# Optimization experiments

Measured on AMD Instinct MI355X. Metric: run time of the kernel, lower is better.

The kernel has to match this reference:

```python
import jax, jax.numpy as jnp
import numpy as np

SCALE_FACTORS = (1, 2, 4)
N, T, F = 4096, 128, 128
MARKET = 64
MIX = sum(T // k for k in SCALE_FACTORS)  # 224


def hardswish(x):
    return x * jnp.clip(x + 3.0, 0.0, 6.0) * (1.0 / 6.0)


def layernorm2d(x, g, b, eps=1e-5):
    # LayerNorm with normalized_shape == last two dims (as in torch nn.LayerNorm((A, B)))
    mu = jnp.mean(x, axis=(-2, -1), keepdims=True)
    var = jnp.var(x, axis=(-2, -1), keepdims=True)
    return (x - mu) * jax.lax.rsqrt(var + eps) * g + b


def setup_inputs() -> dict:
    key = jax.random.key(0)
    ks = jax.random.split(key, 32)
    inp = {"x": jax.random.normal(ks[0], (N, T, F), jnp.float32)}
    i = 1
    for si, k in enumerate(SCALE_FACTORS):
        tk = T // k
        inp[f"cw{si}"] = jax.random.normal(ks[i], (F, F, k), jnp.float32) * 0.05; i += 1
        inp[f"cb{si}"] = jnp.zeros((F,), jnp.float32)
        inp[f"lg{si}"] = jnp.ones((tk, F), jnp.float32)
        inp[f"lb{si}"] = jnp.zeros((tk, F), jnp.float32)
        inp[f"L1_{si}"] = jax.random.normal(ks[i], (tk, tk), jnp.float32) * 0.01; i += 1
        inp[f"L2_{si}"] = jax.random.normal(ks[i], (tk, tk), jnp.float32) * 0.01; i += 1
    inp["fc_w"] = jax.random.normal(ks[i], (1, F), jnp.float32) * 0.05; i += 1
    inp["fc_b"] = jnp.zeros((1,), jnp.float32)
    inp["sm_lg"] = jnp.ones((N, MIX), jnp.float32)
    inp["sm_lb"] = jnp.zeros((N, MIX), jnp.float32)
    inp["M1"] = jax.random.normal(ks[i], (MARKET, N), jnp.float32); i += 1
    inp["M2"] = jax.random.normal(ks[i], (N, MARKET), jnp.float32); i += 1
    inp["sm_fc_w"] = jax.random.normal(ks[i], (1, 2 * MIX), jnp.float32) * 0.02; i += 1
    inp["sm_fc_b"] = jnp.zeros((1,), jnp.float32)
    return inp


def _forward(x, cw0, cb0, lg0, lb0, L1_0, L2_0,
             cw1, cb1, lg1, lb1, L1_1, L2_1,
             cw2, cb2, lg2, lb2, L1_2, L2_2,
             fc_w, fc_b, sm_lg, sm_lb, M1, M2, sm_fc_w, sm_fc_b):
    n, t, f = x.shape
    per_scale = ((cw0, cb0, lg0, lb0, L1_0, L2_0),
                 (cw1, cb1, lg1, lb1, L1_1, L2_1),
                 (cw2, cb2, lg2, lb2, L1_2, L2_2))
    parts = []
    for k, (cw, cb, lg, lb, L1, L2) in zip(SCALE_FACTORS, per_scale):
        tk = t // k
        # Conv1d(kernel=k, stride=k) == blockwise contraction over non-overlapping windows
        xr = x.transpose(0, 2, 1).reshape(n, f, tk, k)          # (n, F_in, tk, k)
        xt = jnp.einsum('nitk,oik->nto', xr, cw) + cb            # (n, tk, F)
        # TimeMixing: ragged prefix loop == single lower-triangular matmul over time
        mask = jnp.tril(jnp.ones((tk, tk), x.dtype))
        h = layernorm2d(xt, lg, lb)
        u = hardswish(jnp.einsum('ts,nsf->ntf', L1 * mask, h))
        v = jnp.einsum('ts,nsf->ntf', L2 * mask, u)
        xt = xt + v
        parts.append(xt @ fc_w[0] + fc_b[0])                     # (n, tk)
    h = jnp.concatenate(parts, axis=1)                           # (n, MIX)
    # StockMixing
    hn = layernorm2d(h, sm_lg, sm_lb)
    z = M2 @ hardswish(M1 @ hn)                                  # (n, MIX)
    out = jnp.concatenate([h, h + z], axis=1)                    # (n, 2*MIX)
    return out @ sm_fc_w[0][:, None] + sm_fc_b                   # (n, 1)


def reference(x, cw0, cb0, lg0, lb0, L1_0, L2_0,
              cw1, cb1, lg1, lb1, L1_1, L2_1,
              cw2, cb2, lg2, lb2, L1_2, L2_2,
              fc_w, fc_b, sm_lg, sm_lb, M1, M2, sm_fc_w, sm_fc_b):
    return _forward(x, cw0, cb0, lg0, lb0, L1_0, L2_0,
                    cw1, cb1, lg1, lb1, L1_1, L2_1,
                    cw2, cb2, lg2, lb2, L1_2, L2_2,
                    fc_w, fc_b, sm_lg, sm_lb, M1, M2, sm_fc_w, sm_fc_b)
```

## Files before the change

### kernel.cpp

```cpp
#include <hip/hip_runtime.h>
#include <stdint.h>

typedef __attribute__((ext_vector_type(8))) short short8;
typedef __attribute__((ext_vector_type(4))) float f32x4;
typedef __attribute__((ext_vector_type(4))) unsigned short us4;

__device__ __forceinline__ unsigned short f2bf(float f) {
  union { float f; unsigned int i; } v; v.f = f;
  unsigned int r = (v.i + 0x7FFFu + ((v.i >> 16) & 1u)) >> 16;
  return (unsigned short)r;
}
__device__ __forceinline__ float hswish(float x) {
  float t = fminf(fmaxf(x + 3.f, 0.f), 6.f);
  return x * t * (1.f / 6.f);
}

__device__ __forceinline__ void cwprep(const float* __restrict__ cw,
                                       unsigned short* __restrict__ dst,
                                       int rel, int k, int NKS) {
  int e = rel & 7;
  int lane = (rel >> 3) & 63;
  int rest = rel >> 9;
  int ksl = rest % NKS, ot = rest / NKS;
  int m = ksl * 32 + (lane >> 4) * 8 + e;
  int o = ot * 16 + (lane & 15);
  int j = m >> 7, i = m & 127;
  dst[rel] = f2bf(cw[(o * 128 + i) * k + j]);
}

__global__ void prep_kernel(const float* __restrict__ cw0,
                            const float* __restrict__ cw1,
                            const float* __restrict__ cw2,
                            unsigned short* __restrict__ cwP0,
                            unsigned short* __restrict__ cwP1,
                            unsigned short* __restrict__ cwP2) {
  int idx = blockIdx.x * 256 + threadIdx.x;
  if (idx < 16384)       cwprep(cw0, cwP0, idx,          1,  4);
  else if (idx < 49152)  cwprep(cw1, cwP1, idx - 16384,  2,  8);
  else if (idx < 114688) cwprep(cw2, cwP2, idx - 49152,  4, 16);
}

__device__ __forceinline__ short8 lfrag(const float* __restrict__ L, int TK,
                                        int srow, int scol) {
  const float4 v0 = *(const float4*)(L + srow * TK + scol);
  const float4 v1 = *(const float4*)(L + srow * TK + scol + 4);
  short8 r;
  r[0] = (scol     <= srow) ? (short)f2bf(v0.x) : (short)0;
  r[1] = (scol + 1 <= srow) ? (short)f2bf(v0.y) : (short)0;
  r[2] = (scol + 2 <= srow) ? (short)f2bf(v0.z) : (short)0;
  r[3] = (scol + 3 <= srow) ? (short)f2bf(v0.w) : (short)0;
  r[4] = (scol + 4 <= srow) ? (short)f2bf(v1.x) : (short)0;
  r[5] = (scol + 5 <= srow) ? (short)f2bf(v1.y) : (short)0;
  r[6] = (scol + 6 <= srow) ? (short)f2bf(v1.z) : (short)0;
  r[7] = (scol + 7 <= srow) ? (short)f2bf(v1.w) : (short)0;
  return r;
}

template <int S, int nTT>
__device__ __forceinline__ void conv_o(const unsigned short* __restrict__ xb,
                                       const unsigned short* __restrict__ cwP,
                                       f32x4 (&acc)[nTT][2],
                                       int wave, int lane, int quad, int l16) {
  constexpr int NKS = (128 << S) / 32;
#pragma unroll
  for (int tt = 0; tt < nTT; ++tt)
#pragma unroll
    for (int oo = 0; oo < 2; ++oo)
      acc[tt][oo] = (f32x4){0.f, 0.f, 0.f, 0.f};

#pragma unroll
  for (int ks = 0; ks < NKS; ++ks) {
    const int m = ks * 32 + quad * 8;
    short8 a[nTT];
#pragma unroll
    for (int tt = 0; tt < nTT; ++tt) {
      int t = tt * 16 + l16;
      a[tt] = *(const short8*)&xb[((t << S) + (m >> 7)) * 136 + (m & 127)];
    }
#pragma unroll
    for (int oo = 0; oo < 2; ++oo) {
      const short8 b = *(const short8*)&cwP[(((wave * 2 + oo) * NKS + ks) * 64 + lane) * 8];
#pragma unroll
      for (int tt = 0; tt < nTT; ++tt)
        acc[tt][oo] = __builtin_amdgcn_mfma_f32_16x16x32_bf16(a[tt], b, acc[tt][oo], 0, 0, 0);
    }
  }
}

template <int S, int nTT>
__device__ __forceinline__ void post_o(unsigned short* __restrict__ HT,
                                       float* __restrict__ scratch,
                                       f32x4 (&acc)[nTT][2],
                                       const float* __restrict__ cb,
                                       const float* __restrict__ lg,
                                       const float* __restrict__ lb,
                                       const float* __restrict__ L1,
                                       const float* __restrict__ L2,
                                       int tid, int wave, int lane,
                                       int quad, int l16) {
  constexpr int TK    = 128 >> S;
  constexpr int OFF   = (S == 0) ? 0 : (S == 1 ? 128 : 192);
  constexpr int NTS   = TK / 32;
  constexpr int HTP   = TK + 8;
  constexpr int nTOwn = (S == 0) ? 2 : 1;
  constexpr int nFF   = (S == 2) ? 4 : 8;
  const int ffBase  = (S == 2) ? ((wave >> 1) * 4) : 0;
  const int maxTown = (S == 0) ? (wave + 4) : ((S == 1) ? wave : (wave & 1));

  float sum = 0.f, ss = 0.f;
#pragma unroll
  for (int oo = 0; oo < 2; ++oo) {
    float cbv = cb[(wave * 2 + oo) * 16 + l16];
#pragma unroll
    for (int tt = 0; tt < nTT; ++tt)
#pragma unroll
      for (int r = 0; r < 4; ++r) {
        float v = acc[tt][oo][r] + cbv;
        acc[tt][oo][r] = v;
        sum += v; ss += v * v;
      }
  }
#pragma unroll
  for (int m = 32; m >= 1; m >>= 1) {
    sum += __shfl_xor(sum, m);
    ss  += __shfl_xor(ss, m);
  }
  if (lane == 0) { scratch[352 + wave * 2] = sum; scratch[353 + wave * 2] = ss; }

#pragma unroll
  for (int tt = 0; tt < nTT; ++tt)
#pragma unroll
    for (int r = 0; r < 4; ++r) {
      float v = acc[tt][0][r] * scratch[(wave * 2) * 16 + l16]
              + acc[tt][1][r] * scratch[(wave * 2 + 1) * 16 + l16];
      v += __shfl_xor(v, 1); v += __shfl_xor(v, 2);
      v += __shfl_xor(v, 4); v += __shfl_xor(v, 8);
      if (l16 == 0)
        atomicAdd(&scratch[128 + OFF + tt * 16 + quad * 4 + r], v);
    }
  __syncthreads();

  const float Sm = scratch[352] + scratch[354] + scratch[356] + scratch[358];
  const float Sq = scratch[353] + scratch[355] + scratch[357] + scratch[359];
  const float mu = Sm * (1.f / (float)(TK * 128));
  const float rsig = rsqrtf(Sq * (1.f / (float)(TK * 128)) - mu * mu + 1e-5f);

#pragma unroll
  for (int oo = 0; oo < 2; ++oo) {
    const int o = (wave * 2 + oo) * 16 + l16;
#pragma unroll
    for (int tt = 0; tt < nTT; ++tt)
#pragma unroll
      for (int r = 0; r < 4; ++r) {
        const int t = tt * 16 + quad * 4 + r;
        float hv = (acc[tt][oo][r] - mu) * rsig * lg[t * 128 + o] + lb[t * 128 + o];
        HT[o * HTP + t] = f2bf(hv);
      }
  }
  __syncthreads();

  f32x4 uacc[nTOwn][nFF];
#pragma unroll
  for (int tt = 0; tt < nTOwn; ++tt)
#pragma unroll
    for (int ff = 0; ff < nFF; ++ff)
      uacc[tt][ff] = (f32x4){0.f, 0.f, 0.f, 0.f};

#pragma unroll
  for (int ks = 0; ks < NTS; ++ks) {
    const int k0 = ks * 32;
    if (k0 <= maxTown * 16 + 15) {
      short8 a[nTOwn];
#pragma unroll
      for (int tt = 0; tt < nTOwn; ++tt) {
        const int tw = (S == 0) ? (wave + tt * 4) : maxTown;
        if (k0 <= tw * 16 + 15)
          a[tt] = lfrag(L1, TK, tw * 16 + l16, k0 + quad * 8);
      }
#pragma unroll
      for (int ff = 0; ff < nFF; ++ff) {
        const short8 b = *(const short8*)&HT[((ffBase + ff) * 16 + l16) * HTP + k0 + quad * 8];
#pragma unroll
        for (int tt = 0; tt < nTOwn; ++tt) {
          const int tw = (S == 0) ? (wave + tt * 4) : maxTown;
          if (k0 <= tw * 16 + 15)
            uacc[tt][ff] = __builtin_amdgcn_mfma_f32_16x16x32_bf16(a[tt], b, uacc[tt][ff], 0, 0, 0);
        }
      }
    }
  }
  __syncthreads();

#pragma unroll
  for (int tt = 0; tt < nTOwn; ++tt) {
    const int tw = (S == 0) ? (wave + tt * 4) : maxTown;
#pragma unroll
    for (int ff = 0; ff < nFF; ++ff) {
      const int f = (ffBase + ff) * 16 + l16;
#pragma unroll
      for (int r = 0; r < 4; ++r) {
        const int t = tw * 16 + quad * 4 + r;
        HT[f * HTP + t] = f2bf(hswish(uacc[tt][ff][r]));
      }
    }
  }
  __syncthreads();

#pragma unroll
  for (int tt = 0; tt < nTOwn; ++tt)
#pragma unroll
    for (int ff = 0; ff < nFF; ++ff)
      uacc[tt][ff] = (f32x4){0.f, 0.f, 0.f, 0.f};

#pragma unroll
  for (int ks = 0; ks < NTS; ++ks) {
    const int k0 = ks * 32;
    if (k0 <= maxTown * 16 + 15) {
      short8 a[nTOwn];
#pragma unroll
      for (int tt = 0; tt < nTOwn; ++tt) {
        const int tw = (S == 0) ? (wave + tt * 4) : maxTown;
        if (k0 <= tw * 16 + 15)
          a[tt] = lfrag(L2, TK, tw * 16 + l16, k0 + quad * 8);
      }
#pragma unroll
      for (int ff = 0; ff < nFF; ++ff) {
        const short8 b = *(const short8*)&HT[((ffBase + ff) * 16 + l16) * HTP + k0 + quad * 8];
#pragma unroll
        for (int tt = 0; tt < nTOwn; ++tt) {
          const int tw = (S == 0) ? (wave + tt * 4) : maxTown;
          if (k0 <= tw * 16 + 15)
            uacc[tt][ff] = __builtin_amdgcn_mfma_f32_16x16x32_bf16(a[tt], b, uacc[tt][ff], 0, 0, 0);
        }
      }
    }
  }

#pragma unroll
  for (int tt = 0; tt < nTOwn; ++tt) {
    const int tw = (S == 0) ? (wave + tt * 4) : maxTown;
#pragma unroll
    for (int r = 0; r < 4; ++r) {
      float v = 0.f;
#pragma unroll
      for (int ff = 0; ff < nFF; ++ff)
        v += uacc[tt][ff][r] * scratch[(ffBase + ff) * 16 + l16];
      v += __shfl_xor(v, 1); v += __shfl_xor(v, 2);
      v += __shfl_xor(v, 4); v += __shfl_xor(v, 8);
      if (l16 == 0)
        atomicAdd(&scratch[128 + OFF + tw * 16 + quad * 4 + r], v);
    }
  }
}

__launch_bounds__(256, 2)
__global__ void s1_fused(const float* __restrict__ x,
                         const float* __restrict__ cb0, const float* __restrict__ lg0,
                         const float* __restrict__ lb0, const float* __restrict__ L1_0,
                         const float* __restrict__ L2_0,
                         const float* __restrict__ cb1, const float* __restrict__ lg1,
                         const float* __restrict__ lb1, const float* __restrict__ L1_1,
                         const float* __restrict__ L2_1,
                         const float* __restrict__ cb2, const float* __restrict__ lg2,
                         const float* __restrict__ lb2, const float* __restrict__ L1_2,
                         const float* __restrict__ L2_2,
                         const float* __restrict__ fc_w, const float* __restrict__ fc_b,
                         const unsigned short* __restrict__ cwP0,
                         const unsigned short* __restrict__ cwP1,
                         const unsigned short* __restrict__ cwP2,
                         float* __restrict__ h_out,
                         float* __restrict__ stats) {
  extern __shared__ char smem[];
  unsigned short* xb = (unsigned short*)smem;
  float* scratch = (float*)(smem + 34816);

  const int tid  = threadIdx.x;
  const int wave = tid >> 6;
  const int lane = tid & 63;
  const int quad = lane >> 4;
  const int l16  = lane & 15;
  const int n    = blockIdx.x;
  const float* xn = x + (size_t)n * 16384;

  if (tid < 128) scratch[tid] = fc_w[tid];
  if (tid < 224) scratch[128 + tid] = 0.f;

  for (int i = tid; i < 4096; i += 256) {
    int t = i >> 5, c4 = (i & 31) * 4;
    const float4 v = *(const float4*)(xn + t * 128 + c4);
    us4 p; p[0] = f2bf(v.x); p[1] = f2bf(v.y); p[2] = f2bf(v.z); p[3] = f2bf(v.w);
    *(us4*)&xb[t * 136 + c4] = p;
  }
  __syncthreads();

  f32x4 acc0[8][2], acc1[4][2], acc2[2][2];
  conv_o<0, 8>(xb, cwP0, acc0, wave, lane, quad, l16);
  conv_o<1, 4>(xb, cwP1, acc1, wave, lane, quad, l16);
  conv_o<2, 2>(xb, cwP2, acc2, wave, lane, quad, l16);

  unsigned short* HT = xb;
  post_o<2, 2>(HT, scratch, acc2, cb2, lg2, lb2, L1_2, L2_2, tid, wave, lane, quad, l16);
  post_o<1, 4>(HT, scratch, acc1, cb1, lg1, lb1, L1_1, L2_1, tid, wave, lane, quad, l16);
  post_o<0, 8>(HT, scratch, acc0, cb0, lg0, lb0, L1_0, L2_0, tid, wave, lane, quad, l16);

  __syncthreads();

  float hv = 0.f;
  if (tid < 224) {
    hv = scratch[128 + tid] + fc_b[0];
    h_out[(size_t)n * 224 + tid] = hv;
  }
  float s = hv, sq = hv * hv;
#pragma unroll
  for (int m = 32; m >= 1; m >>= 1) {
    s  += __shfl_xor(s, m);
    sq += __shfl_xor(sq, m);
  }
  __syncthreads();
  if (lane == 0) { scratch[352 + wave * 2] = s; scratch[353 + wave * 2] = sq; }
  __syncthreads();
  if (tid == 0) {
    atomicAdd(&stats[0], scratch[352] + scratch[354] + scratch[356] + scratch[358]);
    atomicAdd(&stats[1], scratch[353] + scratch[355] + scratch[357] + scratch[359]);
  }
}

__global__ void mix1_kernel(const float* __restrict__ h,
                            const float* __restrict__ sm_lg,
                            const float* __restrict__ sm_lb,
                            const float* __restrict__ M1,
                            const float* __restrict__ stats,
                            float* __restrict__ A) {
  const int m = blockIdx.x;
  const int seg = blockIdx.y;
  const int tid = threadIdx.x;
  const int wave = tid >> 6;
  const int lane = tid & 63;

  __shared__ float tile[2][64 * 65];
  __shared__ float red[256];

  const float inv = 1.f / 917504.f;
  const float mu = stats[0] * inv;
  const float var = stats[1] * inv - mu * mu;
  const float rsig = rsqrtf(var + 1e-5f);

  const int rr = tid >> 2;
  const int cbase = (tid & 3) * 16;

  float acc = 0.f;
  for (int c = 0; c < 16; ++c) {
    const int n0 = seg * 1024 + c * 64;
    float* tl = tile[c & 1];
#pragma unroll
    for (int i = 0; i < 4; ++i) {
      const float4 v = *(const float4*)(M1 + rr * 4096 + n0 + cbase + i * 4);
      tl[rr * 65 + cbase + i * 4    ] = v.x;
      tl[rr * 65 + cbase + i * 4 + 1] = v.y;
      tl[rr * 65 + cbase + i * 4 + 2] = v.z;
      tl[rr * 65 + cbase + i * 4 + 3] = v.w;
    }
    __syncthreads();
#pragma unroll
    for (int j = 0; j < 16; ++j) {
      const int nn = wave * 16 + j;
      const int n = n0 + nn;
      const float hn = (h[n * 224 + m] - mu) * rsig * sm_lg[n * 224 + m] + sm_lb[n * 224 + m];
      acc += tl[lane * 65 + nn] * hn;
    }
  }
  red[tid] = acc;
  __syncthreads();
  if (tid < 64)
    atomicAdd(&A[m * 64 + tid],
              red[tid] + red[64 + tid] + red[128 + tid] + red[192 + tid]);
}

__global__ void out_kernel(const float* __restrict__ h,
                           const float* __restrict__ A,
                           const float* __restrict__ M2,
                           const float* __restrict__ sm_fc_w,
                           const float* __restrict__ sm_fc_b,
                           float* __restrict__ out) {
  const int tid = threadIdx.x;
  const int wave = tid >> 6, lane = tid & 63;
  __shared__ float red[256];
  __shared__ float cv[64];

  {
    const int r = tid & 63, ch = tid >> 6;
    float acc = 0.f;
    for (int j = ch; j < 224; j += 4)
      acc += hswish(A[j * 64 + r]) * sm_fc_w[224 + j];
    red[tid] = acc;
  }
  __syncthreads();
  if (tid < 64)
    cv[tid] = red[tid] + red[64 + tid] + red[128 + tid] + red[192 + tid];
  __syncthreads();

  const int n = blockIdx.x * 4 + wave;
  float acc = M2[n * 64 + lane] * cv[lane];
  for (int j = lane; j < 224; j += 64)
    acc += h[n * 224 + j] * (sm_fc_w[j] + sm_fc_w[224 + j]);
#pragma unroll
  for (int m = 32; m >= 1; m >>= 1) acc += __shfl_xor(acc, m);
  if (lane == 0) out[n] = acc + sm_fc_b[0];
}

extern "C" void kernel_launch(void* const* d_in, const int* in_sizes, int n_in,
                              void* d_out, int out_size, void* d_ws, size_t ws_size,
                              hipStream_t stream) {
  const float* x      = (const float*)d_in[0];
  const float* cw0    = (const float*)d_in[1];
  const float* cb0    = (const float*)d_in[2];
  const float* lg0    = (const float*)d_in[3];
  const float* lb0    = (const float*)d_in[4];
  const float* L1_0   = (const float*)d_in[5];
  const float* L2_0   = (const float*)d_in[6];
  const float* cw1    = (const float*)d_in[7];
  const float* cb1    = (const float*)d_in[8];
  const float* lg1    = (const float*)d_in[9];
  const float* lb1    = (const float*)d_in[10];
  const float* L1_1   = (const float*)d_in[11];
  const float* L2_1   = (const float*)d_in[12];
  const float* cw2    = (const float*)d_in[13];
  const float* cb2    = (const float*)d_in[14];
  const float* lg2    = (const float*)d_in[15];
  const float* lb2    = (const float*)d_in[16];
  const float* L1_2   = (const float*)d_in[17];
  const float* L2_2   = (const float*)d_in[18];
  const float* fc_w   = (const float*)d_in[19];
  const float* fc_b   = (const float*)d_in[20];
  const float* sm_lg  = (const float*)d_in[21];
  const float* sm_lb  = (const float*)d_in[22];
  const float* M1     = (const float*)d_in[23];
  const float* M2     = (const float*)d_in[24];
  const float* sm_fc_w = (const float*)d_in[25];
  const float* sm_fc_b = (const float*)d_in[26];

  char* ws = (char*)d_ws;
  unsigned short* cwP0 = (unsigned short*)(ws);
  unsigned short* cwP1 = (unsigned short*)(ws + 32768);
  unsigned short* cwP2 = (unsigned short*)(ws + 98304);
  float* h     = (float*)(ws + 229376);
  float* stats = (float*)(ws + 3899392);
  float* A     = (float*)(ws + 3899648);

  prep_kernel<<<448, 256, 0, stream>>>(cw0, cw1, cw2, cwP0, cwP1, cwP2);

  hipMemsetAsync(ws + 3899392, 0, 57600, stream);

  constexpr size_t S1_LDS = 34816 + 362 * 4;

  s1_fused<<<4096, 256, S1_LDS, stream>>>(
      x,
      cb0, lg0, lb0, L1_0, L2_0,
      cb1, lg1, lb1, L1_1, L2_1,
      cb2, lg2, lb2, L1_2, L2_2,
      fc_w, fc_b, cwP0, cwP1, cwP2, h, stats);

  mix1_kernel<<<dim3(224, 4), 256, 0, stream>>>(h, sm_lg, sm_lb, M1, stats, A);
  out_kernel<<<1024, 256, 0, stream>>>(h, A, M2, sm_fc_w, sm_fc_b, (float*)d_out);
}
```

Before: 809.0 us.

## Batch all three scales' post-conv stages with separate LDS buffers to cut barriers

Gives each time scale its own LDS buffer, so the three per-scale post-processing chains (layernorm stats, fc partials, two masked time-mixing matmuls) run interleaved and share one barrier per stage instead of one per scale per stage. It also folds the workspace memset into the prep kernel, which removes one launch. In exchange LDS per block grows to about 65KB, which may lower occupancy, and more accumulators stay live at once, which may raise register pressure.

```diff
diff --git a/kernel.cpp b/kernel.cpp
--- a/kernel.cpp
+++ b/kernel.cpp
@@ -33,11 +33,13 @@
                             const float* __restrict__ cw2,
                             unsigned short* __restrict__ cwP0,
                             unsigned short* __restrict__ cwP1,
-                            unsigned short* __restrict__ cwP2) {
+                            unsigned short* __restrict__ cwP2,
+                            float* __restrict__ zeroDst) {
   int idx = blockIdx.x * 256 + threadIdx.x;
   if (idx < 16384)       cwprep(cw0, cwP0, idx,          1,  4);
   else if (idx < 49152)  cwprep(cw1, cwP1, idx - 16384,  2,  8);
   else if (idx < 114688) cwprep(cw2, cwP2, idx - 49152,  4, 16);
+  else if (idx < 129088) zeroDst[idx - 114688] = 0.f;
 }
 
 __device__ __forceinline__ short8 lfrag(const float* __restrict__ L, int TK,
@@ -88,25 +90,11 @@
 }
 
 template <int S, int nTT>
-__device__ __forceinline__ void post_o(unsigned short* __restrict__ HT,
-                                       float* __restrict__ scratch,
-                                       f32x4 (&acc)[nTT][2],
-                                       const float* __restrict__ cb,
-                                       const float* __restrict__ lg,
-                                       const float* __restrict__ lb,
-                                       const float* __restrict__ L1,
-                                       const float* __restrict__ L2,
-                                       int tid, int wave, int lane,
-                                       int quad, int l16) {
-  constexpr int TK    = 128 >> S;
-  constexpr int OFF   = (S == 0) ? 0 : (S == 1 ? 128 : 192);
-  constexpr int NTS   = TK / 32;
-  constexpr int HTP   = TK + 8;
-  constexpr int nTOwn = (S == 0) ? 2 : 1;
-  constexpr int nFF   = (S == 2) ? 4 : 8;
-  const int ffBase  = (S == 2) ? ((wave >> 1) * 4) : 0;
-  const int maxTown = (S == 0) ? (wave + 4) : ((S == 1) ? wave : (wave & 1));
-
+__device__ __forceinline__ void lnfc1(float* __restrict__ scratch,
+                                      f32x4 (&acc)[nTT][2],
+                                      const float* __restrict__ cb,
+                                      int wave, int lane, int quad, int l16) {
+  constexpr int OFF = (S == 0) ? 0 : (S == 1 ? 128 : 192);
   float sum = 0.f, ss = 0.f;
 #pragma unroll
   for (int oo = 0; oo < 2; ++oo) {
@@ -125,8 +113,10 @@
     sum += __shfl_xor(sum, m);
     ss  += __shfl_xor(ss, m);
   }
-  if (lane == 0) { scratch[352 + wave * 2] = sum; scratch[353 + wave * 2] = ss; }
-
+  if (lane == 0) {
+    scratch[352 + S * 8 + wave * 2] = sum;
+    scratch[353 + S * 8 + wave * 2] = ss;
+  }
 #pragma unroll
   for (int tt = 0; tt < nTT; ++tt)
 #pragma unroll
@@ -138,13 +128,23 @@
       if (l16 == 0)
         atomicAdd(&scratch[128 + OFF + tt * 16 + quad * 4 + r], v);
     }
-  __syncthreads();
-
-  const float Sm = scratch[352] + scratch[354] + scratch[356] + scratch[358];
-  const float Sq = scratch[353] + scratch[355] + scratch[357] + scratch[359];
+}
+
+template <int S, int nTT>
+__device__ __forceinline__ void htw(unsigned short* __restrict__ HT,
+                                    const float* __restrict__ scratch,
+                                    f32x4 (&acc)[nTT][2],
+                                    const float* __restrict__ lg,
+                                    const float* __restrict__ lb,
+                                    int wave, int quad, int l16) {
+  constexpr int TK  = 128 >> S;
+  constexpr int HTP = TK + 8;
+  const float Sm = scratch[352 + S * 8] + scratch[354 + S * 8] +
+                   scratch[356 + S * 8] + scratch[358 + S * 8];
+  const float Sq = scratch[353 + S * 8] + scratch[355 + S * 8] +
+                   scratch[357 + S * 8] + scratch[359 + S * 8];
   const float mu = Sm * (1.f / (float)(TK * 128));
   const float rsig = rsqrtf(Sq * (1.f / (float)(TK * 128)) - mu * mu + 1e-5f);
-
 #pragma unroll
   for (int oo = 0; oo < 2; ++oo) {
     const int o = (wave * 2 + oo) * 16 + l16;
@@ -157,15 +157,20 @@
         HT[o * HTP + t] = f2bf(hv);
       }
   }
-  __syncthreads();
-
-  f32x4 uacc[nTOwn][nFF];
-#pragma unroll
-  for (int tt = 0; tt < nTOwn; ++tt)
-#pragma unroll
-    for (int ff = 0; ff < nFF; ++ff)
-      uacc[tt][ff] = (f32x4){0.f, 0.f, 0.f, 0.f};
-
+}
+
+template <int S>
+__device__ __forceinline__ void tmpass(const unsigned short* __restrict__ HT,
+                                       const float* __restrict__ L,
+                                       f32x4 (&u)[(S == 0) ? 2 : 1][(S == 2) ? 4 : 8],
+                                       int wave, int l16, int quad) {
+  constexpr int TK    = 128 >> S;
+  constexpr int NTS   = TK / 32;
+  constexpr int HTP   = TK + 8;
+  constexpr int nTOwn = (S == 0) ? 2 : 1;
+  constexpr int nFF   = (S == 2) ? 4 : 8;
+  const int ffBase  = (S == 2) ? ((wave >> 1) * 4) : 0;
+  const int maxTown = (S == 0) ? (wave + 4) : ((S == 1) ? wave : (wave & 1));
 #pragma unroll
   for (int ks = 0; ks < NTS; ++ks) {
     const int k0 = ks * 32;
@@ -175,7 +180,7 @@
       for (int tt = 0; tt < nTOwn; ++tt) {
         const int tw = (S == 0) ? (wave + tt * 4) : maxTown;
         if (k0 <= tw * 16 + 15)
-          a[tt] = lfrag(L1, TK, tw * 16 + l16, k0 + quad * 8);
+          a[tt] = lfrag(L, TK, tw * 16 + l16, k0 + quad * 8);
       }
 #pragma unroll
       for (int ff = 0; ff < nFF; ++ff) {
@@ -184,13 +189,23 @@
         for (int tt = 0; tt < nTOwn; ++tt) {
           const int tw = (S == 0) ? (wave + tt * 4) : maxTown;
           if (k0 <= tw * 16 + 15)
-            uacc[tt][ff] = __builtin_amdgcn_mfma_f32_16x16x32_bf16(a[tt], b, uacc[tt][ff], 0, 0, 0);
+            u[tt][ff] = __builtin_amdgcn_mfma_f32_16x16x32_bf16(a[tt], b, u[tt][ff], 0, 0, 0);
         }
       }
     }
   }
-  __syncthreads();
-
+}
+
+template <int S>
+__device__ __forceinline__ void utw(unsigned short* __restrict__ HT,
+                                    f32x4 (&u)[(S == 0) ? 2 : 1][(S == 2) ? 4 : 8],
+                                    int wave, int l16, int quad) {
+  constexpr int TK    = 128 >> S;
+  constexpr int HTP   = TK + 8;
+  constexpr int nTOwn = (S == 0) ? 2 : 1;
+  constexpr int nFF   = (S == 2) ? 4 : 8;
+  const int ffBase  = (S == 2) ? ((wave >> 1) * 4) : 0;
+  const int maxTown = (S == 0) ? (wave + 4) : ((S == 1) ? wave : (wave & 1));
 #pragma unroll
   for (int tt = 0; tt < nTOwn; ++tt) {
     const int tw = (S == 0) ? (wave + tt * 4) : maxTown;
@@ -200,42 +215,21 @@
 #pragma unroll
       for (int r = 0; r < 4; ++r) {
         const int t = tw * 16 + quad * 4 + r;
-        HT[f * HTP + t] = f2bf(hswish(uacc[tt][ff][r]));
+        HT[f * HTP + t] = f2bf(hswish(u[tt][ff][r]));
       }
     }
   }
-  __syncthreads();
-
-#pragma unroll
-  for (int tt = 0; tt < nTOwn; ++tt)
-#pragma unroll
-    for (int ff = 0; ff < nFF; ++ff)
-      uacc[tt][ff] = (f32x4){0.f, 0.f, 0.f, 0.f};
-
-#pragma unroll
-  for (int ks = 0; ks < NTS; ++ks) {
-    const int k0 = ks * 32;
-    if (k0 <= maxTown * 16 + 15) {
-      short8 a[nTOwn];
-#pragma unroll
-      for (int tt = 0; tt < nTOwn; ++tt) {
-        const int tw = (S == 0) ? (wave + tt * 4) : maxTown;
-        if (k0 <= tw * 16 + 15)
-          a[tt] = lfrag(L2, TK, tw * 16 + l16, k0 + quad * 8);
-      }
-#pragma unroll
-      for (int ff = 0; ff < nFF; ++ff) {
-        const short8 b = *(const short8*)&HT[((ffBase + ff) * 16 + l16) * HTP + k0 + quad * 8];
-#pragma unroll
-        for (int tt = 0; tt < nTOwn; ++tt) {
-          const int tw = (S == 0) ? (wave + tt * 4) : maxTown;
-          if (k0 <= tw * 16 + 15)
-            uacc[tt][ff] = __builtin_amdgcn_mfma_f32_16x16x32_bf16(a[tt], b, uacc[tt][ff], 0, 0, 0);
-        }
-      }
-    }
-  }
-
+}
+
+template <int S>
+__device__ __forceinline__ void fc2(float* __restrict__ scratch,
+                                    f32x4 (&u)[(S == 0) ? 2 : 1][(S == 2) ? 4 : 8],
+                                    int wave, int l16, int quad) {
+  constexpr int OFF   = (S == 0) ? 0 : (S == 1 ? 128 : 192);
+  constexpr int nTOwn = (S == 0) ? 2 : 1;
+  constexpr int nFF   = (S == 2) ? 4 : 8;
+  const int ffBase  = (S == 2) ? ((wave >> 1) * 4) : 0;
+  const int maxTown = (S == 0) ? (wave + 4) : ((S == 1) ? wave : (wave & 1));
 #pragma unroll
   for (int tt = 0; tt < nTOwn; ++tt) {
     const int tw = (S == 0) ? (wave + tt * 4) : maxTown;
@@ -244,7 +238,7 @@
       float v = 0.f;
 #pragma unroll
       for (int ff = 0; ff < nFF; ++ff)
-        v += uacc[tt][ff][r] * scratch[(ffBase + ff) * 16 + l16];
+        v += u[tt][ff][r] * scratch[(ffBase + ff) * 16 + l16];
       v += __shfl_xor(v, 1); v += __shfl_xor(v, 2);
       v += __shfl_xor(v, 4); v += __shfl_xor(v, 8);
       if (l16 == 0)
@@ -271,8 +265,10 @@
                          float* __restrict__ h_out,
                          float* __restrict__ stats) {
   extern __shared__ char smem[];
-  unsigned short* xb = (unsigned short*)smem;
-  float* scratch = (float*)(smem + 34816);
+  unsigned short* xb  = (unsigned short*)smem;
+  unsigned short* HT1 = (unsigned short*)(smem + 34816);
+  unsigned short* HT2 = (unsigned short*)(smem + 53248);
+  float* scratch      = (float*)(smem + 63488);
 
   const int tid  = threadIdx.x;
   const int wave = tid >> 6;
@@ -298,11 +294,51 @@
   conv_o<1, 4>(xb, cwP1, acc1, wave, lane, quad, l16);
   conv_o<2, 2>(xb, cwP2, acc2, wave, lane, quad, l16);
 
-  unsigned short* HT = xb;
-  post_o<2, 2>(HT, scratch, acc2, cb2, lg2, lb2, L1_2, L2_2, tid, wave, lane, quad, l16);
-  post_o<1, 4>(HT, scratch, acc1, cb1, lg1, lb1, L1_1, L2_1, tid, wave, lane, quad, l16);
-  post_o<0, 8>(HT, scratch, acc0, cb0, lg0, lb0, L1_0, L2_0, tid, wave, lane, quad, l16);
-
+  lnfc1<0, 8>(scratch, acc0, cb0, wave, lane, quad, l16);
+  lnfc1<1, 4>(scratch, acc1, cb1, wave, lane, quad, l16);
+  lnfc1<2, 2>(scratch, acc2, cb2, wave, lane, quad, l16);
+  __syncthreads();
+
+  htw<0, 8>(xb,  scratch, acc0, lg0, lb0, wave, quad, l16);
+  htw<1, 4>(HT1, scratch, acc1, lg1, lb1, wave, quad, l16);
+  htw<2, 2>(HT2, scratch, acc2, lg2, lb2, wave, quad, l16);
+  __syncthreads();
+
+  f32x4 u0[2][8], u1[1][8], u2[1][4];
+#pragma unroll
+  for (int t = 0; t < 2; ++t)
+#pragma unroll
+    for (int f = 0; f < 8; ++f) u0[t][f] = (f32x4){0.f, 0.f, 0.f, 0.f};
+#pragma unroll
+  for (int f = 0; f < 8; ++f) u1[0][f] = (f32x4){0.f, 0.f, 0.f, 0.f};
+#pragma unroll
+  for (int f = 0; f < 4; ++f) u2[0][f] = (f32x4){0.f, 0.f, 0.f, 0.f};
+
+  tmpass<0>(xb,  L1_0, u0, wave, l16, quad);
+  tmpass<1>(HT1, L1_1, u1, wave, l16, quad);
+  tmpass<2>(HT2, L1_2, u2, wave, l16, quad);
+  __syncthreads();
+
+  utw<0>(xb,  u0, wave, l16, quad);
+  utw<1>(HT1, u1, wave, l16, quad);
+  utw<2>(HT2, u2, wave, l16, quad);
+  __syncthreads();
+
+#pragma unroll
+  for (int t = 0; t < 2; ++t)
+#pragma unroll
+    for (int f = 0; f < 8; ++f) u0[t][f] = (f32x4){0.f, 0.f, 0.f, 0.f};
+#pragma unroll
+  for (int f = 0; f < 8; ++f) u1[0][f] = (f32x4){0.f, 0.f, 0.f, 0.f};
+#pragma unroll
+  for (int f = 0; f < 4; ++f) u2[0][f] = (f32x4){0.f, 0.f, 0.f, 0.f};
+
+  tmpass<0>(xb,  L2_0, u0, wave, l16, quad);
+  tmpass<1>(HT1, L2_1, u1, wave, l16, quad);
+  tmpass<2>(HT2, L2_2, u2, wave, l16, quad);
+  fc2<0>(scratch, u0, wave, l16, quad);
+  fc2<1>(scratch, u1, wave, l16, quad);
+  fc2<2>(scratch, u2, wave, l16, quad);
   __syncthreads();
 
   float hv = 0.f;
@@ -316,7 +352,6 @@
     s  += __shfl_xor(s, m);
     sq += __shfl_xor(sq, m);
   }
-  __syncthreads();
   if (lane == 0) { scratch[352 + wave * 2] = s; scratch[353 + wave * 2] = sq; }
   __syncthreads();
   if (tid == 0) {
@@ -447,11 +482,9 @@
   float* stats = (float*)(ws + 3899392);
   float* A     = (float*)(ws + 3899648);
 
-  prep_kernel<<<448, 256, 0, stream>>>(cw0, cw1, cw2, cwP0, cwP1, cwP2);
-
-  hipMemsetAsync(ws + 3899392, 0, 57600, stream);
-
-  constexpr size_t S1_LDS = 34816 + 362 * 4;
+  prep_kernel<<<505, 256, 0, stream>>>(cw0, cw1, cw2, cwP0, cwP1, cwP2, stats);
+
+  constexpr size_t S1_LDS = 64992;
 
   s1_fused<<<4096, 256, S1_LDS, stream>>>(
       x,
```

Result: no change. 812.4 us (+0.4%).

## Read x directly from global in conv, interleave conv/post per scale, fold memset into prep

Applied to the files above, without the earlier changes.

The conv stage now loads fp32 x straight from global memory and converts it to bf16 per MFMA fragment, instead of staging the whole tile in LDS first. Each scale's conv and post-processing now run back to back, so only one accumulator set is live at a time, and launch bounds are raised to target 4 blocks per CU. The separate memset is folded into the prep kernel and one barrier is removed. The trade-off is redundant global reads of x across scales and waves (the conv for k=2 and k=4 re-reads the same rows) in exchange for lower LDS and register pressure and higher occupancy.

```diff
diff --git a/kernel.cpp b/kernel.cpp
--- a/kernel.cpp
+++ b/kernel.cpp
@@ -33,11 +33,13 @@
                             const float* __restrict__ cw2,
                             unsigned short* __restrict__ cwP0,
                             unsigned short* __restrict__ cwP1,
-                            unsigned short* __restrict__ cwP2) {
+                            unsigned short* __restrict__ cwP2,
+                            float* __restrict__ zeroDst) {
   int idx = blockIdx.x * 256 + threadIdx.x;
   if (idx < 16384)       cwprep(cw0, cwP0, idx,          1,  4);
   else if (idx < 49152)  cwprep(cw1, cwP1, idx - 16384,  2,  8);
   else if (idx < 114688) cwprep(cw2, cwP2, idx - 49152,  4, 16);
+  else if (idx < 129088) zeroDst[idx - 114688] = 0.f;
 }
 
 __device__ __forceinline__ short8 lfrag(const float* __restrict__ L, int TK,
@@ -57,7 +59,7 @@
 }
 
 template <int S, int nTT>
-__device__ __forceinline__ void conv_o(const unsigned short* __restrict__ xb,
+__device__ __forceinline__ void conv_g(const float* __restrict__ xn,
                                        const unsigned short* __restrict__ cwP,
                                        f32x4 (&acc)[nTT][2],
                                        int wave, int lane, int quad, int l16) {
@@ -71,11 +73,20 @@
 #pragma unroll
   for (int ks = 0; ks < NKS; ++ks) {
     const int m = ks * 32 + quad * 8;
+    const int row_off = m >> 7, col = m & 127;
     short8 a[nTT];
 #pragma unroll
     for (int tt = 0; tt < nTT; ++tt) {
-      int t = tt * 16 + l16;
-      a[tt] = *(const short8*)&xb[((t << S) + (m >> 7)) * 136 + (m & 127)];
+      const int t = tt * 16 + l16;
+      const float* p = xn + ((t << S) + row_off) * 128 + col;
+      const float4 v0 = *(const float4*)(p);
+      const float4 v1 = *(const float4*)(p + 4);
+      short8 av;
+      av[0] = (short)f2bf(v0.x); av[1] = (short)f2bf(v0.y);
+      av[2] = (short)f2bf(v0.z); av[3] = (short)f2bf(v0.w);
+      av[4] = (short)f2bf(v1.x); av[5] = (short)f2bf(v1.y);
+      av[6] = (short)f2bf(v1.z); av[7] = (short)f2bf(v1.w);
+      a[tt] = av;
     }
 #pragma unroll
     for (int oo = 0; oo < 2; ++oo) {
@@ -253,7 +264,7 @@
   }
 }
 
-__launch_bounds__(256, 2)
+__launch_bounds__(256, 4)
 __global__ void s1_fused(const float* __restrict__ x,
                          const float* __restrict__ cb0, const float* __restrict__ lg0,
                          const float* __restrict__ lb0, const float* __restrict__ L1_0,
@@ -271,7 +282,7 @@
                          float* __restrict__ h_out,
                          float* __restrict__ stats) {
   extern __shared__ char smem[];
-  unsigned short* xb = (unsigned short*)smem;
+  unsigned short* HT = (unsigned short*)smem;
   float* scratch = (float*)(smem + 34816);
 
   const int tid  = threadIdx.x;
@@ -284,24 +295,23 @@
 
   if (tid < 128) scratch[tid] = fc_w[tid];
   if (tid < 224) scratch[128 + tid] = 0.f;
-
-  for (int i = tid; i < 4096; i += 256) {
-    int t = i >> 5, c4 = (i & 31) * 4;
-    const float4 v = *(const float4*)(xn + t * 128 + c4);
-    us4 p; p[0] = f2bf(v.x); p[1] = f2bf(v.y); p[2] = f2bf(v.z); p[3] = f2bf(v.w);
-    *(us4*)&xb[t * 136 + c4] = p;
-  }
-  __syncthreads();
-
-  f32x4 acc0[8][2], acc1[4][2], acc2[2][2];
-  conv_o<0, 8>(xb, cwP0, acc0, wave, lane, quad, l16);
-  conv_o<1, 4>(xb, cwP1, acc1, wave, lane, quad, l16);
-  conv_o<2, 2>(xb, cwP2, acc2, wave, lane, quad, l16);
-
-  unsigned short* HT = xb;
-  post_o<2, 2>(HT, scratch, acc2, cb2, lg2, lb2, L1_2, L2_2, tid, wave, lane, quad, l16);
-  post_o<1, 4>(HT, scratch, acc1, cb1, lg1, lb1, L1_1, L2_1, tid, wave, lane, quad, l16);
-  post_o<0, 8>(HT, scratch, acc0, cb0, lg0, lb0, L1_0, L2_0, tid, wave, lane, quad, l16);
+  __syncthreads();
+
+  {
+    f32x4 acc[8][2];
+    conv_g<0, 8>(xn, cwP0, acc, wave, lane, quad, l16);
+    post_o<0, 8>(HT, scratch, acc, cb0, lg0, lb0, L1_0, L2_0, tid, wave, lane, quad, l16);
+  }
+  {
+    f32x4 acc[4][2];
+    conv_g<1, 4>(xn, cwP1, acc, wave, lane, quad, l16);
+    post_o<1, 4>(HT, scratch, acc, cb1, lg1, lb1, L1_1, L2_1, tid, wave, lane, quad, l16);
+  }
+  {
+    f32x4 acc[2][2];
+    conv_g<2, 2>(xn, cwP2, acc, wave, lane, quad, l16);
+    post_o<2, 2>(HT, scratch, acc, cb2, lg2, lb2, L1_2, L2_2, tid, wave, lane, quad, l16);
+  }
 
   __syncthreads();
 
@@ -316,7 +326,6 @@
     s  += __shfl_xor(s, m);
     sq += __shfl_xor(sq, m);
   }
-  __syncthreads();
   if (lane == 0) { scratch[352 + wave * 2] = s; scratch[353 + wave * 2] = sq; }
   __syncthreads();
   if (tid == 0) {
@@ -447,11 +456,9 @@
   float* stats = (float*)(ws + 3899392);
   float* A     = (float*)(ws + 3899648);
 
-  prep_kernel<<<448, 256, 0, stream>>>(cw0, cw1, cw2, cwP0, cwP1, cwP2);
-
-  hipMemsetAsync(ws + 3899392, 0, 57600, stream);
-
-  constexpr size_t S1_LDS = 34816 + 362 * 4;
+  prep_kernel<<<505, 256, 0, stream>>>(cw0, cw1, cw2, cwP0, cwP1, cwP2, stats);
+
+  constexpr size_t S1_LDS = 34816 + 376 * 4;
 
   s1_fused<<<4096, 256, S1_LDS, stream>>>(
       x,
```

Result: slower. 1.085 ms (+34.1%).
